# Kernel tuning notes

Hardware: AMD Instinct MI355X
Metric: run time of the kernel (lower is better)

## Reference

```python
import jax, jax.numpy as jnp
import numpy as np

N = 100000
E = 1600000
HID = 128


def gcn_conv(x, W, b, src, dst, n):
    # PyG GCNConv: h = X W; add self-loops; D^{-1/2}(A+I)D^{-1/2} h + b
    h = x @ W                                   # [n, out]
    loop = jnp.arange(n)
    s = jnp.concatenate([src, loop])            # sources incl. self-loops
    d = jnp.concatenate([dst, loop])            # targets incl. self-loops
    deg = jax.ops.segment_sum(jnp.ones(s.shape[0], dtype=h.dtype), d, num_segments=n)
    dinv = jnp.where(deg > 0, jax.lax.rsqrt(deg), 0.0)
    norm = dinv[s] * dinv[d]                    # [E+n]
    out = jax.ops.segment_sum(h[s] * norm[:, None], d, num_segments=n)
    return out + b


def setup_inputs() -> dict:
    key = jax.random.key(0)
    ks = jax.random.split(key, 16)
    coords = jax.random.normal(ks[0], (N, 2), dtype=jnp.float32)
    edge_index = jax.random.randint(ks[1], (2, E), 0, N, dtype=jnp.int64)

    def lin(k, fin, fout):
        k1, k2 = jax.random.split(k)
        s = 1.0 / np.sqrt(fin)
        W = jax.random.uniform(k1, (fin, fout), jnp.float32, -s, s)
        b = jax.random.uniform(k2, (fout,), jnp.float32, -s, s)
        return W, b

    W1, b1 = lin(ks[2], 3, HID)
    W2, b2 = lin(ks[3], HID, HID)
    Ws, bs = lin(ks[4], HID, 1)
    Wmu, bmu = lin(ks[5], HID, 2)
    Wls, bls = lin(ks[6], HID, 2)
    Wv1, bv1 = lin(ks[7], HID, 64)
    Wv2, bv2 = lin(ks[8], 64, 1)
    return {"coords": coords, "edge_index": edge_index,
            "W1": W1, "b1": b1, "W2": W2, "b2": b2,
            "Ws": Ws, "bs": bs, "Wmu": Wmu, "bmu": bmu,
            "Wls": Wls, "bls": bls, "Wv1": Wv1, "bv1": bv1,
            "Wv2": Wv2, "bv2": bv2}


def reference(coords, edge_index, W1, b1, W2, b2, Ws, bs, Wmu, bmu, Wls, bls, Wv1, bv1, Wv2, bv2):
    n = coords.shape[0]
    src, dst = edge_index[0], edge_index[1]
    # degree feature (no self-loops), normalized by max degree
    degree = jax.ops.segment_sum(jnp.ones(src.shape[0], dtype=jnp.float32), src, num_segments=n)
    degree = degree / jnp.maximum(degree.max(), 1.0)
    x = jnp.concatenate([coords, degree[:, None]], axis=1)  # [N, 3]
    x = jax.nn.relu(gcn_conv(x, W1, b1, src, dst, n))       # [N, HID]
    x = jax.nn.relu(gcn_conv(x, W2, b2, src, dst, n))       # [N, HID]
    node_logits = jax.nn.log_softmax((x @ Ws + bs).squeeze(-1), axis=0)  # [N]
    mu = x @ Wmu + bmu                                      # [N, 2]
    log_std = jnp.clip(x @ Wls + bls, -4.0, 2.0)            # [N, 2]
    g = x.mean(axis=0)                                      # [HID]
    value = (jax.nn.relu(g @ Wv1 + bv1) @ Wv2 + bv2).squeeze()
    return node_logits, mu, log_std, value
```

## Files before the change

kernel.cpp:

```cpp
#include <hip/hip_runtime.h>
#include <hip/hip_bf16.h>

#define HID 128
#define NB2MAX 128

typedef __bf16 bf16x8 __attribute__((ext_vector_type(8)));
typedef float f32x4 __attribute__((ext_vector_type(4)));
typedef float f32x2 __attribute__((ext_vector_type(2)));

#if defined(__has_builtin)
#if __has_builtin(__builtin_amdgcn_cvt_pk_f32_fp8) && __has_builtin(__builtin_amdgcn_cvt_pk_fp8_f32)
#define HAVE_FP8_CVT 1
#endif
#endif
#ifndef HAVE_FP8_CVT
#define HAVE_FP8_CVT 0
#include <hip/hip_fp8.h>
#endif

__device__ __forceinline__ float b2f(unsigned int u) { return __uint_as_float(u << 16); }
__device__ __forceinline__ unsigned int f2b(float f) {
  unsigned int b = __float_as_uint(f);
  return (b + 0x7FFFu + ((b >> 16) & 1u)) >> 16;
}
__device__ __forceinline__ unsigned int pack2(float lo, float hi) {
  return f2b(lo) | (f2b(hi) << 16);
}

#if !HAVE_FP8_CVT
__device__ __forceinline__ float fp8dec(unsigned int u) {
  unsigned int e = (u >> 3) & 15, m = u & 7, sgn = (u >> 7) & 1;
  float v;
  if (e) v = __uint_as_float(((e + 120) << 23) | (m << 20));
  else v = (float)m * 0.001953125f;
  return sgn ? -v : v;
}
#endif

__device__ __forceinline__ unsigned int pk4_fp8(float v0, float v1, float v2, float v3) {
#if HAVE_FP8_CVT
  int pk = 0;
  pk = __builtin_amdgcn_cvt_pk_fp8_f32(v0, v1, pk, false);
  pk = __builtin_amdgcn_cvt_pk_fp8_f32(v2, v3, pk, true);
  return (unsigned int)pk;
#else
  __hip_fp8_e4m3 a(v0), b(v1), c(v2), d(v3);
  return (unsigned)a.__x | ((unsigned)b.__x << 8) | ((unsigned)c.__x << 16) |
         ((unsigned)d.__x << 24);
#endif
}

__device__ __forceinline__ void acc4_fp8(unsigned int u, float* a) {
#if HAVE_FP8_CVT
  f32x2 lo = __builtin_amdgcn_cvt_pk_f32_fp8((int)u, false);
  f32x2 hi = __builtin_amdgcn_cvt_pk_f32_fp8((int)u, true);
  a[0] += lo.x; a[1] += lo.y; a[2] += hi.x; a[3] += hi.y;
#else
  a[0] += fp8dec(u & 255); a[1] += fp8dec((u >> 8) & 255);
  a[2] += fp8dec((u >> 16) & 255); a[3] += fp8dec((u >> 24) & 255);
#endif
}

__global__ void k_scatter2(const int* __restrict__ src, const int* __restrict__ dst, int E,
                           int NB2, int CAP, int* __restrict__ curd, int* __restrict__ curs,
                           int* __restrict__ pairsp, unsigned short* __restrict__ srcb) {
  __shared__ int hd[NB2MAX], hs[NB2MAX], bd[NB2MAX], bs[NB2MAX];
  for (int i = threadIdx.x; i < NB2; i += 256) { hd[i] = 0; hs[i] = 0; }
  __syncthreads();
  int per = (E + gridDim.x - 1) / gridDim.x;
  int begin = blockIdx.x * per;
  int end = min(E, begin + per);
  for (int e = begin + threadIdx.x; e < end; e += 256) {
    atomicAdd(&hd[dst[e] >> 10], 1);
    atomicAdd(&hs[src[e] >> 10], 1);
  }
  __syncthreads();
  for (int i = threadIdx.x; i < NB2; i += 256) {
    bd[i] = hd[i] ? atomicAdd(&curd[i], hd[i]) : 0;
    bs[i] = hs[i] ? atomicAdd(&curs[i], hs[i]) : 0;
    hd[i] = 0; hs[i] = 0;
  }
  __syncthreads();
  for (int e = begin + threadIdx.x; e < end; e += 256) {
    int d = dst[e], s = src[e];
    int bD = d >> 10, bS = s >> 10;
    int offD = bd[bD] + atomicAdd(&hd[bD], 1);
    if (offD < CAP) pairsp[(size_t)bD * CAP + offD] = (s << 10) | (d & 1023);
    int offS = bs[bS] + atomicAdd(&hs[bS], 1);
    if (offS < CAP) srcb[(size_t)bS * CAP + offS] = (unsigned short)(s & 1023);
  }
}

__global__ __launch_bounds__(1024) void k_degcsr(
    const unsigned short* __restrict__ srcb, const int* __restrict__ curs,
    const int* __restrict__ pairsp, const int* __restrict__ curd, int NB2, int CAP, int N,
    int* __restrict__ degsrc, int* __restrict__ bmax, int2* __restrict__ rowptr2,
    float* __restrict__ dinv, int* __restrict__ colarr,
    const float* __restrict__ W2, unsigned short* __restrict__ W2T) {
  __shared__ int cnt[1024], scn[1024], cur[1024];
  int tid = threadIdx.x;
  if ((int)blockIdx.x >= 2 * NB2) {
    int idx = (blockIdx.x - 2 * NB2) * 1024 + tid;
    if (idx < 128 * 128) {
      int j = idx >> 7, k = idx & 127;
      W2T[j * 128 + k] = (unsigned short)f2b(W2[k * 128 + j]);
    }
    return;
  }
  if ((int)blockIdx.x < NB2) {
    int b = blockIdx.x;
    int g = (b << 10) + tid;
    int lo = b * CAP;
    cnt[tid] = 0; __syncthreads();
    int szS = min(curs[b], CAP);
    const unsigned short* sb = srcb + (size_t)lo;
    for (int k = tid; k < szS; k += 1024) atomicAdd(&cnt[sb[k]], 1);
    __syncthreads();
    int c = cnt[tid];
    if (g < N) degsrc[g] = c;
    scn[tid] = (g < N) ? c : 0; __syncthreads();
    for (int s = 512; s > 0; s >>= 1) {
      if (tid < s) scn[tid] = max(scn[tid], scn[tid + s]);
      __syncthreads();
    }
    if (tid == 0) bmax[b] = scn[0];
    return;
  }
  int b = blockIdx.x - NB2;
  int g = (b << 10) + tid;
  int lo = b * CAP;
  cnt[tid] = 0; __syncthreads();
  int szD = min(curd[b], CAP);
  const int* pb = pairsp + (size_t)lo;
  for (int k = tid; k < szD; k += 1024) atomicAdd(&cnt[pb[k] & 1023], 1);
  __syncthreads();
  int c = cnt[tid];
  scn[tid] = c; __syncthreads();
  for (int st = 1; st < 1024; st <<= 1) {
    int t = (tid >= st) ? scn[tid - st] : 0;
    __syncthreads();
    scn[tid] += t;
    __syncthreads();
  }
  int excl = scn[tid] - c;
  if (g < N) {
    rowptr2[g] = make_int2(lo + excl, lo + excl + c);
    dinv[g] = rsqrtf((float)(c + 1));
  }
  cur[tid] = lo + excl;
  __syncthreads();
  for (int k = tid; k < szD; k += 1024) {
    int p = pb[k];
    int pos = atomicAdd(&cur[p & 1023], 1);
    colarr[pos] = ((unsigned)p) >> 10;
  }
}

__global__ void k_node(const float* __restrict__ coords, const int* __restrict__ degsrc,
                       const float* __restrict__ dinv, const int* __restrict__ bmax, int NB2,
                       int N, float4* __restrict__ x0s) {
  __shared__ int sm[128];
  int tid = threadIdx.x;
  if (tid < 128) sm[tid] = (tid < NB2) ? bmax[tid] : 0;
  __syncthreads();
  if (tid < 64) { sm[tid] = max(sm[tid], sm[tid + 64]); }
  __syncthreads();
  if (tid < 32) { sm[tid] = max(sm[tid], sm[tid + 32]); }
  __syncthreads();
  if (tid < 16) { sm[tid] = max(sm[tid], sm[tid + 16]); }
  __syncthreads();
  if (tid < 8) { sm[tid] = max(sm[tid], sm[tid + 8]); }
  __syncthreads();
  if (tid < 4) { sm[tid] = max(sm[tid], sm[tid + 4]); }
  __syncthreads();
  if (tid < 2) { sm[tid] = max(sm[tid], sm[tid + 2]); }
  __syncthreads();
  if (tid == 0) sm[0] = max(sm[0], sm[1]);
  __syncthreads();
  float inv = 1.0f / (float)max(sm[0], 1);
  int n = blockIdx.x * 256 + tid;
  if (n >= N) return;
  float di = dinv[n];
  float4 v;
  v.x = coords[n * 2 + 0] * di;
  v.y = coords[n * 2 + 1] * di;
  v.z = (float)degsrc[n] * inv * di;
  v.w = 0.f;
  x0s[n] = v;
}

__global__ void k_agg3lin(const float4* __restrict__ x0s, const float* __restrict__ dinv,
                          const int2* __restrict__ rowptr2, const int* __restrict__ col,
                          const float* __restrict__ W1, const float* __restrict__ b1, int N,
                          unsigned int* __restrict__ x1f8) {
  __shared__ float w0s[128], w1s[128], w2s[128], bsm[128];
  for (int t = threadIdx.x; t < 128; t += 256) {
    w0s[t] = W1[t];
    w1s[t] = W1[128 + t];
    w2s[t] = W1[256 + t];
    bsm[t] = b1[t];
  }
  __syncthreads();
  int n = blockIdx.x * 256 + threadIdx.x;
  if (n >= N) return;
  float4 a = x0s[n];
  int2 rp = rowptr2[n];
  int k = rp.x, en = rp.y;
  for (; k + 3 < en; k += 4) {
    int s0 = col[k], s1 = col[k + 1], s2 = col[k + 2], s3 = col[k + 3];
    float4 w0 = x0s[s0];
    float4 w1 = x0s[s1];
    float4 w2 = x0s[s2];
    float4 w3 = x0s[s3];
    a.x += (w0.x + w1.x) + (w2.x + w3.x);
    a.y += (w0.y + w1.y) + (w2.y + w3.y);
    a.z += (w0.z + w1.z) + (w2.z + w3.z);
  }
  for (; k < en; k++) {
    float4 w = x0s[col[k]];
    a.x += w.x; a.y += w.y; a.z += w.z;
  }
  float di = dinv[n];
  float ax = a.x * di, ay = a.y * di, az = a.z * di;
  unsigned int* orow = x1f8 + (size_t)n * 32;
#pragma unroll 8
  for (int f0 = 0; f0 < 128; f0 += 4) {
    float v0 = fmaxf(bsm[f0] + ax * w0s[f0] + ay * w1s[f0] + az * w2s[f0], 0.f) * di;
    float v1 = fmaxf(bsm[f0 + 1] + ax * w0s[f0 + 1] + ay * w1s[f0 + 1] + az * w2s[f0 + 1], 0.f) * di;
    float v2 = fmaxf(bsm[f0 + 2] + ax * w0s[f0 + 2] + ay * w1s[f0 + 2] + az * w2s[f0 + 2], 0.f) * di;
    float v3 = fmaxf(bsm[f0 + 3] + ax * w0s[f0 + 3] + ay * w1s[f0 + 3] + az * w2s[f0 + 3], 0.f) * di;
    orow[f0 >> 2] = pk4_fp8(v0, v1, v2, v3);
  }
}

__global__ void k_agg128(const unsigned int* __restrict__ x1f8, const float* __restrict__ dinv,
                         const int2* __restrict__ rowptr2, const int* __restrict__ col,
                         int N, unsigned short* __restrict__ xa) {
  int g = (int)((blockIdx.x * 256 + threadIdx.x) >> 3);
  int lane = threadIdx.x & 7;
  if (g >= N) return;
  const uint4* base = (const uint4*)x1f8 + lane;
  float acc[16];
#pragma unroll
  for (int i = 0; i < 16; i++) acc[i] = 0.f;
  uint4 self = base[(size_t)g * 8];
  acc4_fp8(self.x, acc); acc4_fp8(self.y, acc + 4);
  acc4_fp8(self.z, acc + 8); acc4_fp8(self.w, acc + 12);
  int2 rp = rowptr2[g];
  int k = rp.x, en = rp.y;
  for (; k + 3 < en; k += 4) {
    int s0 = col[k], s1 = col[k + 1], s2 = col[k + 2], s3 = col[k + 3];
    uint4 w0 = base[(size_t)s0 * 8];
    uint4 w1 = base[(size_t)s1 * 8];
    uint4 w2 = base[(size_t)s2 * 8];
    uint4 w3 = base[(size_t)s3 * 8];
    acc4_fp8(w0.x, acc); acc4_fp8(w0.y, acc + 4); acc4_fp8(w0.z, acc + 8); acc4_fp8(w0.w, acc + 12);
    acc4_fp8(w1.x, acc); acc4_fp8(w1.y, acc + 4); acc4_fp8(w1.z, acc + 8); acc4_fp8(w1.w, acc + 12);
    acc4_fp8(w2.x, acc); acc4_fp8(w2.y, acc + 4); acc4_fp8(w2.z, acc + 8); acc4_fp8(w2.w, acc + 12);
    acc4_fp8(w3.x, acc); acc4_fp8(w3.y, acc + 4); acc4_fp8(w3.z, acc + 8); acc4_fp8(w3.w, acc + 12);
  }
  for (; k < en; k++) {
    uint4 w = base[(size_t)col[k] * 8];
    acc4_fp8(w.x, acc); acc4_fp8(w.y, acc + 4); acc4_fp8(w.z, acc + 8); acc4_fp8(w.w, acc + 12);
  }
  float di = dinv[g];
  uint4 o1, o2;
  o1.x = pack2(acc[0] * di, acc[1] * di);
  o1.y = pack2(acc[2] * di, acc[3] * di);
  o1.z = pack2(acc[4] * di, acc[5] * di);
  o1.w = pack2(acc[6] * di, acc[7] * di);
  o2.x = pack2(acc[8] * di, acc[9] * di);
  o2.y = pack2(acc[10] * di, acc[11] * di);
  o2.z = pack2(acc[12] * di, acc[13] * di);
  o2.w = pack2(acc[14] * di, acc[15] * di);
  uint4* op = (uint4*)xa + (size_t)g * 16 + lane * 2;
  op[0] = o1;
  op[1] = o2;
}

__global__ __launch_bounds__(256) void k_gemm2(const unsigned short* __restrict__ xab,
                                               const unsigned short* __restrict__ W2T,
                                               const float* __restrict__ b2,
                                               const float* __restrict__ Ws,
                                               const float* __restrict__ bs,
                                               const float* __restrict__ Wmu,
                                               const float* __restrict__ bmu,
                                               const float* __restrict__ Wls,
                                               const float* __restrict__ bls,
                                               int N, float* __restrict__ s_arr,
                                               float* __restrict__ out,
                                               float* __restrict__ partials) {
  __shared__ float w[640];
  __shared__ float cs[4][128];
  for (int t = threadIdx.x; t < 128; t += 256) {
    w[t] = Ws[t];
    w[128 + t] = Wmu[t * 2 + 0];
    w[256 + t] = Wmu[t * 2 + 1];
    w[384 + t] = Wls[t * 2 + 0];
    w[512 + t] = Wls[t * 2 + 1];
  }
  __syncthreads();
  int wv = threadIdx.x >> 6;
  int lane = threadIdx.x & 63;
  int l15 = lane & 15, lhi = lane >> 4;
  int rowbase = blockIdx.x * 64 + wv * 16;
  int arow = rowbase + l15;
  int arowc = min(arow, N - 1);
  const unsigned short* ap = xab + (size_t)arowc * HID + lhi * 8;
  bf16x8 a[4];
#pragma unroll
  for (int kk = 0; kk < 4; kk++) a[kk] = *(const bf16x8*)(ap + kk * 32);
  float cpart[8];
  float p0[4] = {0, 0, 0, 0}, p1[4] = {0, 0, 0, 0}, p2[4] = {0, 0, 0, 0};
  float p3[4] = {0, 0, 0, 0}, p4[4] = {0, 0, 0, 0};
#pragma unroll
  for (int ct = 0; ct < 8; ct++) {
    f32x4 acc = {0.f, 0.f, 0.f, 0.f};
    const unsigned short* bp = W2T + (size_t)(ct * 16 + l15) * HID + lhi * 8;
#pragma unroll
    for (int kk = 0; kk < 4; kk++) {
      bf16x8 bfr = *(const bf16x8*)(bp + kk * 32);
      acc = __builtin_amdgcn_mfma_f32_16x16x32_bf16(a[kk], bfr, acc, 0, 0, 0);
    }
    int cidx = ct * 16 + l15;
    float bias = b2[cidx];
    float ws_ = w[cidx];
    float wm0 = w[128 + cidx], wm1 = w[256 + cidx];
    float wl0 = w[384 + cidx], wl1 = w[512 + cidx];
    float cl = 0.f;
#pragma unroll
    for (int r = 0; r < 4; r++) {
      int node = rowbase + lhi * 4 + r;
      float o = fmaxf(acc[r] + bias, 0.f);
      if (node < N) cl += o;
      p0[r] += o * ws_;
      p1[r] += o * wm0;
      p2[r] += o * wm1;
      p3[r] += o * wl0;
      p4[r] += o * wl1;
    }
    cl += __shfl_xor(cl, 16);
    cl += __shfl_xor(cl, 32);
    cpart[ct] = cl;
  }
#pragma unroll
  for (int r = 0; r < 4; r++) {
#pragma unroll
    for (int m = 1; m < 16; m <<= 1) {
      p0[r] += __shfl_xor(p0[r], m);
      p1[r] += __shfl_xor(p1[r], m);
      p2[r] += __shfl_xor(p2[r], m);
      p3[r] += __shfl_xor(p3[r], m);
      p4[r] += __shfl_xor(p4[r], m);
    }
  }
  if (l15 == 0) {
#pragma unroll
    for (int r = 0; r < 4; r++) {
      int node = rowbase + lhi * 4 + r;
      if (node < N) {
        s_arr[node] = p0[r] + bs[0];
        out[(size_t)N + node * 2 + 0] = p1[r] + bmu[0];
        out[(size_t)N + node * 2 + 1] = p2[r] + bmu[1];
        out[(size_t)3 * N + node * 2 + 0] = fminf(fmaxf(p3[r] + bls[0], -4.f), 2.f);
        out[(size_t)3 * N + node * 2 + 1] = fminf(fmaxf(p4[r] + bls[1], -4.f), 2.f);
      }
    }
  }
  if (lane < 16) {
#pragma unroll
    for (int ct = 0; ct < 8; ct++) cs[wv][ct * 16 + lane] = cpart[ct];
  }
  __syncthreads();
  if (threadIdx.x < 128) {
    int f = threadIdx.x;
    partials[(size_t)blockIdx.x * 128 + f] = cs[0][f] + cs[1][f] + cs[2][f] + cs[3][f];
  }
}

__global__ void k_lse_colsum(const float* __restrict__ s, int N, float* __restrict__ pm,
                             float* __restrict__ pt, const float* __restrict__ partials,
                             int nblkG, float* __restrict__ colsum) {
  if (blockIdx.x >= 256) {
    int bb = blockIdx.x - 256;
    int f = threadIdx.x;
    if (f < 128) {
      float t = 0.f;
      for (int b = bb; b < nblkG; b += 64) t += partials[(size_t)b * 128 + f];
      atomicAdd(&colsum[f], t);
    }
    return;
  }
  __shared__ float smM[256], smT[256];
  float m = -1e30f, t = 0.f;
  for (int i = blockIdx.x * 256 + threadIdx.x; i < N; i += 256 * 256) {
    float v = s[i];
    if (v > m) { t = t * __expf(m - v) + 1.f; m = v; }
    else t += __expf(v - m);
  }
  smM[threadIdx.x] = m; smT[threadIdx.x] = t; __syncthreads();
  for (int st = 128; st > 0; st >>= 1) {
    if (threadIdx.x < st) {
      float m2 = smM[threadIdx.x + st], t2 = smT[threadIdx.x + st];
      float m1 = smM[threadIdx.x], t1 = smT[threadIdx.x];
      float M = fmaxf(m1, m2);
      smM[threadIdx.x] = M;
      smT[threadIdx.x] = t1 * __expf(m1 - M) + t2 * __expf(m2 - M);
    }
    __syncthreads();
  }
  if (threadIdx.x == 0) { pm[blockIdx.x] = smM[0]; pt[blockIdx.x] = smT[0]; }
}

__global__ void k_logits_value(const float* __restrict__ sarr, const float* __restrict__ pm,
                               const float* __restrict__ pt, int N, float* __restrict__ out,
                               const float* __restrict__ colsum, const float* __restrict__ Wv1,
                               const float* __restrict__ bv1, const float* __restrict__ Wv2,
                               const float* __restrict__ bv2, int nblkN) {
  if ((int)blockIdx.x == nblkN) {
    __shared__ float hid[64];
    float invN = 1.0f / (float)N;
    int j = threadIdx.x;
    if (j < 64) {
      float a = bv1[j];
      for (int f = 0; f < 128; f++) a += (colsum[f] * invN) * Wv1[f * 64 + j];
      hid[j] = fmaxf(a, 0.f) * Wv2[j];
    }
    __syncthreads();
    if (threadIdx.x == 0) {
      float v = bv2[0];
      for (int jj = 0; jj < 64; jj++) v += hid[jj];
      out[(size_t)5 * N] = v;
    }
    return;
  }
  __shared__ float smM[256], smT[256];
  smM[threadIdx.x] = pm[threadIdx.x];
  smT[threadIdx.x] = pt[threadIdx.x];
  __syncthreads();
  for (int st = 128; st > 0; st >>= 1) {
    if (threadIdx.x < st) {
      float m2 = smM[threadIdx.x + st], t2 = smT[threadIdx.x + st];
      float m1 = smM[threadIdx.x], t1 = smT[threadIdx.x];
      float M = fmaxf(m1, m2);
      smM[threadIdx.x] = M;
      smT[threadIdx.x] = t1 * __expf(m1 - M) + t2 * __expf(m2 - M);
    }
    __syncthreads();
  }
  float lse = smM[0] + logf(smT[0]);
  int n = blockIdx.x * 256 + threadIdx.x;
  if (n < N) out[n] = sarr[n] - lse;
}

extern "C" void kernel_launch(void* const* d_in, const int* in_sizes, int n_in,
                              void* d_out, int out_size, void* d_ws, size_t ws_size,
                              hipStream_t stream) {
  const float* coords = (const float*)d_in[0];
  const int* ei = (const int*)d_in[1];
  const float* W1 = (const float*)d_in[2];
  const float* b1 = (const float*)d_in[3];
  const float* W2 = (const float*)d_in[4];
  const float* b2 = (const float*)d_in[5];
  const float* Wsw = (const float*)d_in[6];
  const float* bsw = (const float*)d_in[7];
  const float* Wmu = (const float*)d_in[8];
  const float* bmu = (const float*)d_in[9];
  const float* Wls = (const float*)d_in[10];
  const float* bls = (const float*)d_in[11];
  const float* Wv1 = (const float*)d_in[12];
  const float* bv1 = (const float*)d_in[13];
  const float* Wv2 = (const float*)d_in[14];
  const float* bv2 = (const float*)d_in[15];
  int N = in_sizes[0] / 2;
  int E = in_sizes[1] / 2;
  const int* src = ei;
  const int* dst = ei + E;
  float* outf = (float*)d_out;
  int NB2 = (N + 1023) >> 10;
  int CAP = ((E / NB2) * 5 / 4 + 1024 + 255) & ~255;
  int nblkG = (N + 63) / 64;
  int nblkN = (N + 255) / 256;

  char* base = (char*)d_ws;
  size_t off = 0;
  auto alloc = [&](size_t bytes) -> void* {
    void* r = base + off;
    off += (bytes + 255) & ~(size_t)255;
    return r;
  };
  size_t zero_start = off;
  int* curd = (int*)alloc((size_t)NB2 * 4);
  int* curs = (int*)alloc((size_t)NB2 * 4);
  float* colsum = (float*)alloc(128 * 4);
  size_t zero_bytes = off - zero_start;
  int* bmax = (int*)alloc((size_t)NB2 * 4);
  int2* rowptr2 = (int2*)alloc((size_t)N * 8);
  int* pairsp = (int*)alloc((size_t)NB2 * CAP * 4);
  unsigned short* srcb = (unsigned short*)alloc((size_t)NB2 * CAP * 2);
  int* colarr = (int*)alloc((size_t)NB2 * CAP * 4);
  int* degsrc = (int*)alloc((size_t)N * 4);
  float* dinv = (float*)alloc((size_t)N * 4);
  float4* x0s = (float4*)alloc((size_t)N * 16);
  float* sarr = (float*)alloc((size_t)N * 4);
  float* pm = (float*)alloc(256 * 4);
  float* pt = (float*)alloc(256 * 4);
  unsigned short* W2T = (unsigned short*)alloc(128 * 128 * 2);
  float* partials = (float*)alloc((size_t)nblkG * 128 * 4);
  unsigned int* x1f8 = (unsigned int*)alloc((size_t)N * 128);
  unsigned short* xab = (unsigned short*)alloc((size_t)N * HID * 2);
  if (off > ws_size) return;

  hipMemsetAsync(base + zero_start, 0, zero_bytes, stream);
  k_scatter2<<<512, 256, 0, stream>>>(src, dst, E, NB2, CAP, curd, curs, pairsp, srcb);
  k_degcsr<<<2 * NB2 + 16, 1024, 0, stream>>>(srcb, curs, pairsp, curd, NB2, CAP, N, degsrc,
                                              bmax, rowptr2, dinv, colarr, W2, W2T);
  k_node<<<nblkN, 256, 0, stream>>>(coords, degsrc, dinv, bmax, NB2, N, x0s);
  k_agg3lin<<<nblkN, 256, 0, stream>>>(x0s, dinv, rowptr2, colarr, W1, b1, N, x1f8);
  k_agg128<<<(N * 8 + 255) / 256, 256, 0, stream>>>(x1f8, dinv, rowptr2, colarr, N, xab);
  k_gemm2<<<nblkG, 256, 0, stream>>>(xab, W2T, b2, Wsw, bsw, Wmu, bmu, Wls, bls, N, sarr, outf,
                                     partials);
  k_lse_colsum<<<320, 256, 0, stream>>>(sarr, N, pm, pt, partials, nblkG, colsum);
  k_logits_value<<<nblkN + 1, 256, 0, stream>>>(sarr, pm, pt, N, outf, colsum, Wv1, bv1, Wv2,
                                                bv2, nblkN);
}
```

Before: 163.3 us.

## Pad per-block bucket reservations to aligned chunks and use wave-shuffle scans

In the scatter kernel, each block now reserves bucket space rounded up to 16 (dst pairs) or 32 (src shorts) entries and fills the unused slots with sentinel values. The aim is to keep each block's global writes in aligned, full-line chunks. The CSR/degree kernel skips the sentinels, and its LDS tree reductions and scans are replaced by wavefront shuffle scans plus a 16-entry cross-wave combine, which cuts many __syncthreads. In exchange, CAP grows to hold the padding, the degree kernel reads more entries, and the scatter kernel gains a serial padding-fill loop.

```diff
diff --git a/kernel.cpp b/kernel.cpp
--- a/kernel.cpp
+++ b/kernel.cpp
@@ -76,8 +76,9 @@
   }
   __syncthreads();
   for (int i = threadIdx.x; i < NB2; i += 256) {
-    bd[i] = hd[i] ? atomicAdd(&curd[i], hd[i]) : 0;
-    bs[i] = hs[i] ? atomicAdd(&curs[i], hs[i]) : 0;
+    int cd = hd[i], cs_ = hs[i];
+    bd[i] = cd ? atomicAdd(&curd[i], (cd + 15) & ~15) : 0;
+    bs[i] = cs_ ? atomicAdd(&curs[i], (cs_ + 31) & ~31) : 0;
     hd[i] = 0; hs[i] = 0;
   }
   __syncthreads();
@@ -89,6 +90,19 @@
     int offS = bs[bS] + atomicAdd(&hs[bS], 1);
     if (offS < CAP) srcb[(size_t)bS * CAP + offS] = (unsigned short)(s & 1023);
   }
+  __syncthreads();
+  for (int i = threadIdx.x; i < NB2; i += 256) {
+    int cd = hd[i], rd = (cd + 15) & ~15;
+    for (int j = cd; j < rd; j++) {
+      int pos = bd[i] + j;
+      if (pos < CAP) pairsp[(size_t)i * CAP + pos] = -1;
+    }
+    int cs_ = hs[i], rs = (cs_ + 31) & ~31;
+    for (int j = cs_; j < rs; j++) {
+      int pos = bs[i] + j;
+      if (pos < CAP) srcb[(size_t)i * CAP + pos] = 0xFFFFu;
+    }
+  }
 }
 
 __global__ __launch_bounds__(1024) void k_degcsr(
@@ -97,7 +111,8 @@
     int* __restrict__ degsrc, int* __restrict__ bmax, int2* __restrict__ rowptr2,
     float* __restrict__ dinv, int* __restrict__ colarr,
     const float* __restrict__ W2, unsigned short* __restrict__ W2T) {
-  __shared__ int cnt[1024], scn[1024], cur[1024];
+  __shared__ int cnt[1024], cur[1024];
+  __shared__ int wsum[16];
   int tid = threadIdx.x;
   if ((int)blockIdx.x >= 2 * NB2) {
     int idx = (blockIdx.x - 2 * NB2) * 1024 + tid;
@@ -114,16 +129,23 @@
     cnt[tid] = 0; __syncthreads();
     int szS = min(curs[b], CAP);
     const unsigned short* sb = srcb + (size_t)lo;
-    for (int k = tid; k < szS; k += 1024) atomicAdd(&cnt[sb[k]], 1);
+    for (int k = tid; k < szS; k += 1024) {
+      unsigned int v = sb[k];
+      if (v < 1024u) atomicAdd(&cnt[v], 1);
+    }
     __syncthreads();
     int c = cnt[tid];
     if (g < N) degsrc[g] = c;
-    scn[tid] = (g < N) ? c : 0; __syncthreads();
-    for (int s = 512; s > 0; s >>= 1) {
-      if (tid < s) scn[tid] = max(scn[tid], scn[tid + s]);
-      __syncthreads();
-    }
-    if (tid == 0) bmax[b] = scn[0];
+    int m = (g < N) ? c : 0;
+    for (int d = 32; d > 0; d >>= 1) m = max(m, __shfl_xor(m, d));
+    if ((tid & 63) == 0) wsum[tid >> 6] = m;
+    __syncthreads();
+    if (tid == 0) {
+      int mm = 0;
+#pragma unroll
+      for (int i = 0; i < 16; i++) mm = max(mm, wsum[i]);
+      bmax[b] = mm;
+    }
     return;
   }
   int b = blockIdx.x - NB2;
@@ -132,17 +154,31 @@
   cnt[tid] = 0; __syncthreads();
   int szD = min(curd[b], CAP);
   const int* pb = pairsp + (size_t)lo;
-  for (int k = tid; k < szD; k += 1024) atomicAdd(&cnt[pb[k] & 1023], 1);
+  for (int k = tid; k < szD; k += 1024) {
+    int p = pb[k];
+    if (p != -1) atomicAdd(&cnt[p & 1023], 1);
+  }
   __syncthreads();
   int c = cnt[tid];
-  scn[tid] = c; __syncthreads();
-  for (int st = 1; st < 1024; st <<= 1) {
-    int t = (tid >= st) ? scn[tid - st] : 0;
-    __syncthreads();
-    scn[tid] += t;
-    __syncthreads();
-  }
-  int excl = scn[tid] - c;
+  int lane = tid & 63, wid = tid >> 6;
+  int sv = c;
+  for (int d = 1; d < 64; d <<= 1) {
+    int t = __shfl_up(sv, d);
+    if (lane >= d) sv += t;
+  }
+  if (lane == 63) wsum[wid] = sv;
+  __syncthreads();
+  if (tid < 16) {
+    int w = wsum[tid];
+    for (int d = 1; d < 16; d <<= 1) {
+      int t = __shfl_up(w, d, 16);
+      if (tid >= d) w += t;
+    }
+    wsum[tid] = w;
+  }
+  __syncthreads();
+  int incl = sv + (wid ? wsum[wid - 1] : 0);
+  int excl = incl - c;
   if (g < N) {
     rowptr2[g] = make_int2(lo + excl, lo + excl + c);
     dinv[g] = rsqrtf((float)(c + 1));
@@ -151,6 +187,7 @@
   __syncthreads();
   for (int k = tid; k < szD; k += 1024) {
     int p = pb[k];
+    if (p == -1) continue;
     int pos = atomicAdd(&cur[p & 1023], 1);
     colarr[pos] = ((unsigned)p) >> 10;
   }
@@ -478,7 +515,7 @@
   const int* dst = ei + E;
   float* outf = (float*)d_out;
   int NB2 = (N + 1023) >> 10;
-  int CAP = ((E / NB2) * 5 / 4 + 1024 + 255) & ~255;
+  int CAP = ((E / NB2) * 5 / 4 + 512 * 32 + 1024 + 255) & ~255;
   int nblkG = (N + 63) / 64;
   int nblkN = (N + 255) / 256;
 
```

Result: slower. 168.9 us (+3.4%).
